# Optimization experiments

Measured on AMD Instinct MI355X. Metric: run time of the kernel, lower is better.

The kernel has to match this reference:

```python
import jax, jax.numpy as jnp
import numpy as np

B, C, H, W = 4, 256, 64, 64
C8 = C // 8


def setup_inputs() -> dict:
    key = jax.random.key(0)
    ks = jax.random.split(key, 8)
    x = jax.random.normal(ks[0], (B, C, H, W), dtype=jnp.float32)
    valid = jax.random.uniform(ks[1], (B, 1, H, W), dtype=jnp.float32)
    # 1x1 conv weights (kernel_size=1 -> plain channel matmul) + biases
    Wq = jax.random.normal(ks[2], (C8, C), dtype=jnp.float32) * 0.05
    bq = jnp.zeros((C8,), dtype=jnp.float32)
    Wk = jax.random.normal(ks[3], (C8, C), dtype=jnp.float32) * 0.05
    bk = jnp.zeros((C8,), dtype=jnp.float32)
    Wv = jax.random.normal(ks[4], (C, C), dtype=jnp.float32) * 0.05
    bv = jnp.zeros((C,), dtype=jnp.float32)
    gamma = jnp.asarray(0.5, dtype=jnp.float32)  # nonzero so attention path matters
    return {"x": x, "valid": valid, "Wq": Wq, "bq": bq, "Wk": Wk, "bk": bk,
            "Wv": Wv, "bv": bv, "gamma": gamma}


def reference(x, valid, Wq, bq, Wk, bk, Wv, bv, gamma):
    b, c, h, w = x.shape
    n = h * w
    xf = x.reshape(b, c, n)                                   # [B,C,N]
    # valid is already at (H,W): nearest interpolate to same size is identity
    v = valid.reshape(b, 1, n)                                # [B,1,N]
    q = jnp.einsum('oc,bcn->bno', Wq, xf) + bq                # [B,N,C//8]
    k = jnp.einsum('oc,bcn->bon', Wk, xf) + bk[None, :, None] # [B,C//8,N]
    energy = jnp.einsum('bno,bom->bnm', q, k)                 # [B,N,N]
    attn = jax.nn.softmax(energy, axis=-1)
    va = attn * v                                             # mask columns
    scale = 1.0 / jnp.sum(va, axis=2, keepdims=True)          # per-row renorm
    sa = va * scale                                           # [B,N,N]
    pv = jnp.einsum('oc,bcn->bon', Wv, xf) + bv[None, :, None]  # [B,C,N]
    out = jnp.einsum('bon,bmn->bom', pv, sa)                  # bmm(V, A^T)
    out = out.reshape(b, c, h, w)
    return gamma * out + x, sa
```

## Files before the change

kernel.cpp:

```cpp
#include <hip/hip_runtime.h>

typedef unsigned short u16;
typedef unsigned int u32;
typedef __attribute__((ext_vector_type(8))) short short8;
typedef __attribute__((ext_vector_type(4))) float f32x4;
typedef __attribute__((ext_vector_type(2))) unsigned int u32x2;
typedef __attribute__((ext_vector_type(4))) unsigned int u32x4;

#define BB 4
#define CC 256
#define NT 4096
#define L2E 1.4426950408889634f

__device__ __forceinline__ float b2f(u16 v) {
    union { u32 u; float f; } c; c.u = ((u32)v) << 16; return c.f;
}
__device__ __forceinline__ u16 f2b(float f) {
    union { float f; u32 u; } c; c.f = f;
    u32 u = c.u;
    return (u16)((u + 0x7fffu + ((u >> 16) & 1u)) >> 16);
}

__global__ __launch_bounds__(256) void kproj(
    const float* __restrict__ x,
    const float* __restrict__ Wq, const float* __restrict__ bq,
    const float* __restrict__ Wk, const float* __restrict__ bk,
    const float* __restrict__ Wv, const float* __restrict__ bv,
    u16* __restrict__ qh, u16* __restrict__ ql,
    u16* __restrict__ kh, u16* __restrict__ kl,
    u16* __restrict__ pvw)
{
    __shared__ __align__(16) float lA[32][68];
    __shared__ __align__(16) float lX[32][68];
    const int mt = blockIdx.x, nt = blockIdx.y, b = blockIdx.z;
    const int t = threadIdx.x;
    const int tx = t & 15, ty = t >> 4;
    const int n0 = nt * 64;

    float acc[4][4];
    #pragma unroll
    for (int i = 0; i < 4; ++i)
        #pragma unroll
        for (int j = 0; j < 4; ++j) acc[i][j] = 0.f;

    const int rA = t >> 2, kqA = (t & 3) * 8;
    const int rgA = mt * 64 + rA;
    const float* wrow;
    if (rgA < 32)      wrow = Wq + rgA * 256;
    else if (rgA < 64) wrow = Wk + (rgA - 32) * 256;
    else               wrow = Wv + (rgA - 64) * 256;
    const int kX = t >> 3, nn8 = (t & 7) * 8;
    const float* xrow = x + ((size_t)(b * CC + kX)) * NT + n0 + nn8;

    for (int k0 = 0; k0 < 256; k0 += 32) {
        f32x4 wa = *(const f32x4*)(wrow + k0 + kqA);
        f32x4 wb = *(const f32x4*)(wrow + k0 + kqA + 4);
        f32x4 xa = *(const f32x4*)(xrow + (size_t)k0 * NT);
        f32x4 xb = *(const f32x4*)(xrow + (size_t)k0 * NT + 4);
        __syncthreads();
        #pragma unroll
        for (int j = 0; j < 4; ++j) {
            lA[kqA + j    ][rA] = wa[j];
            lA[kqA + j + 4][rA] = wb[j];
        }
        *(f32x4*)&lX[kX][nn8]     = xa;
        *(f32x4*)&lX[kX][nn8 + 4] = xb;
        __syncthreads();
        #pragma unroll
        for (int k = 0; k < 32; ++k) {
            f32x4 av  = *(const f32x4*)&lA[k][ty * 4];
            f32x4 xvv = *(const f32x4*)&lX[k][tx * 4];
            #pragma unroll
            for (int i = 0; i < 4; ++i)
                #pragma unroll
                for (int j = 0; j < 4; ++j)
                    acc[i][j] = fmaf(av[i], xvv[j], acc[i][j]);
        }
    }

    #pragma unroll
    for (int i = 0; i < 4; ++i) {
        const int rg = mt * 64 + ty * 4 + i;
        float bias;
        if (rg < 32)      bias = bq[rg];
        else if (rg < 64) bias = bk[rg - 32];
        else              bias = bv[rg - 64];
        #pragma unroll
        for (int j = 0; j < 4; ++j) {
            const int n = n0 + tx * 4 + j;
            const float val = acc[i][j] + bias;
            const u16 h = f2b(val);
            const u16 l = f2b(val - b2f(h));
            if (rg < 32) {
                const size_t idx = ((size_t)(b * NT + n)) * 32 + rg;
                qh[idx] = h; ql[idx] = l;
            } else if (rg < 64) {
                const size_t idx = ((size_t)(b * NT + n)) * 32 + (rg - 32);
                kh[idx] = h; kl[idx] = l;
            } else {
                pvw[((size_t)b * CC + (rg - 64)) * NT + n] = f2b(val);
            }
        }
    }
}

__global__ __launch_bounds__(256) void kattn(
    const u16* __restrict__ qh, const u16* __restrict__ ql,
    const u16* __restrict__ kh, const u16* __restrict__ kl,
    const float* __restrict__ valid, float* __restrict__ sa)
{
    __shared__ float sred[4][4][4];
    const int b    = blockIdx.y;
    const int lane = threadIdx.x & 63;
    const int wv   = threadIdx.x >> 6;
    const int r0   = blockIdx.x * 16;
    const int quad = lane >> 4, l16 = lane & 15;
    const int ct0  = wv * 64;

    const size_t abase = ((size_t)(b * NT + r0 + l16)) * 32 + quad * 8;
    const short8 aqh = *(const short8*)(qh + abase);
    const short8 aql = *(const short8*)(ql + abase);
    const size_t kb = (size_t)b * NT * 32 + (size_t)l16 * 32 + quad * 8;
    const float* vb = valid + b * NT + l16;
    const f32x4 zero = {0.f, 0.f, 0.f, 0.f};

    float sacc[4] = {0.f, 0.f, 0.f, 0.f};
    for (int ct = ct0; ct < ct0 + 64; ++ct) {
        short8 bh = *(const short8*)(kh + kb + (size_t)ct * 512);
        short8 bl = *(const short8*)(kl + kb + (size_t)ct * 512);
        float vcol = vb[ct * 16];
        f32x4 d = __builtin_amdgcn_mfma_f32_16x16x32_bf16(aqh, bh, zero, 0, 0, 0);
        d = __builtin_amdgcn_mfma_f32_16x16x32_bf16(aql, bh, d, 0, 0, 0);
        d = __builtin_amdgcn_mfma_f32_16x16x32_bf16(aqh, bl, d, 0, 0, 0);
        #pragma unroll
        for (int i = 0; i < 4; ++i)
            sacc[i] += vcol * exp2f(fminf(d[i], 60.f) * L2E);
    }
    #pragma unroll
    for (int i = 0; i < 4; ++i) {
        #pragma unroll
        for (int off = 1; off < 16; off <<= 1)
            sacc[i] += __shfl_xor(sacc[i], off, 64);
    }
    if (l16 == 0) {
        #pragma unroll
        for (int i = 0; i < 4; ++i) sred[wv][quad][i] = sacc[i];
    }
    __syncthreads();
    float inv[4];
    #pragma unroll
    for (int i = 0; i < 4; ++i)
        inv[i] = 1.0f / (sred[0][quad][i] + sred[1][quad][i] +
                         sred[2][quad][i] + sred[3][quad][i]);

    for (int ct = ct0; ct < ct0 + 64; ++ct) {
        short8 bh = *(const short8*)(kh + kb + (size_t)ct * 512);
        short8 bl = *(const short8*)(kl + kb + (size_t)ct * 512);
        float vcol = vb[ct * 16];
        f32x4 d = __builtin_amdgcn_mfma_f32_16x16x32_bf16(aqh, bh, zero, 0, 0, 0);
        d = __builtin_amdgcn_mfma_f32_16x16x32_bf16(aql, bh, d, 0, 0, 0);
        d = __builtin_amdgcn_mfma_f32_16x16x32_bf16(aqh, bl, d, 0, 0, 0);
        #pragma unroll
        for (int i = 0; i < 4; ++i) {
            float val = vcol * exp2f(fminf(d[i], 60.f) * L2E) * inv[i];
            sa[((size_t)(b * NT + r0 + quad * 4 + i)) * NT + ct * 16 + l16] = val;
        }
    }
}

#define KOUT_BODY(CUR, T, NXA, NXB, FTA, FTB)                                  \
  {                                                                            \
    if ((T) + 2 < 32) {                                                        \
      FTA = *(const f32x4*)(sap + (size_t)((T) + 2) * 128);                    \
      FTB = *(const f32x4*)(sap + (size_t)((T) + 2) * 128 + 4);                \
    }                                                                          \
    if ((T) + 1 < 32) {                                                        \
      u32 w0 = (u32)f2b(NXA[0]) | ((u32)f2b(NXA[1]) << 16);                    \
      u32 w1 = (u32)f2b(NXA[2]) | ((u32)f2b(NXA[3]) << 16);                    \
      u32 w2 = (u32)f2b(NXB[0]) | ((u32)f2b(NXB[1]) << 16);                    \
      u32 w3 = (u32)f2b(NXB[2]) | ((u32)f2b(NXB[3]) << 16);                    \
      u32x4 pk = {w0, w1, w2, w3};                                             \
      *(u32x4*)(lbw + ((((T) + 1) & 1) * 8192)) = pk;                          \
    }                                                                          \
    const char* lb = lbr + (CUR) * 8192;                                       \
    _Pragma("unroll")                                                          \
    for (int kk = 0; kk < 128; kk += 32) {                                     \
      short8 a0 = *(const short8*)(a0p + (size_t)(T) * 128 + kk);              \
      short8 a1 = *(const short8*)(a1p + (size_t)(T) * 128 + kk);              \
      const int kby = (((kk + quad * 8) * 2) ^ swz);                           \
      short8 b0 = *(const short8*)(lb + l16 * 256 + kby);                      \
      short8 b1 = *(const short8*)(lb + (16 + l16) * 256 + kby);               \
      acc00 = __builtin_amdgcn_mfma_f32_16x16x32_bf16(a0, b0, acc00, 0, 0, 0); \
      acc01 = __builtin_amdgcn_mfma_f32_16x16x32_bf16(a0, b1, acc01, 0, 0, 0); \
      acc10 = __builtin_amdgcn_mfma_f32_16x16x32_bf16(a1, b0, acc10, 0, 0, 0); \
      acc11 = __builtin_amdgcn_mfma_f32_16x16x32_bf16(a1, b1, acc11, 0, 0, 0); \
    }                                                                          \
    asm volatile("s_waitcnt lgkmcnt(0)" ::: "memory");                         \
    __builtin_amdgcn_sched_barrier(0);                                         \
    __builtin_amdgcn_s_barrier();                                              \
    __builtin_amdgcn_sched_barrier(0);                                         \
  }

__global__ __launch_bounds__(512) void kout(
    const u16* __restrict__ pvw, const float* __restrict__ sa,
    const float* __restrict__ x, const float* __restrict__ gamma,
    float* __restrict__ outp)
{
    __shared__ __align__(16) u16 lB[2][32][128];
    const int b    = blockIdx.y;
    const int m0   = blockIdx.x * 32;
    const int t    = threadIdx.x;
    const int lane = t & 63;
    const int wv   = t >> 6;
    const int c0   = wv * 32;
    const int quad = lane >> 4, l16 = lane & 15;
    const int swz  = (l16 & 7) << 4;

    const u16* a0p = pvw + ((size_t)(b * CC + c0 + l16)) * NT + quad * 8;
    const u16* a1p = a0p + (size_t)16 * NT;
    const int sm = t >> 4, sk = (t & 15) * 8;
    const float* sap = sa + ((size_t)(b * NT + m0 + sm)) * NT + sk;
    char* lbw = ((char*)&lB[0][0][0]) + sm * 256 + ((sk * 2) ^ ((sm & 7) << 4));
    const char* lbr = (const char*)&lB[0][0][0];

    f32x4 acc00 = {0,0,0,0}, acc01 = {0,0,0,0}, acc10 = {0,0,0,0}, acc11 = {0,0,0,0};

    f32x4 pA = *(const f32x4*)(sap);
    f32x4 pB = *(const f32x4*)(sap + 4);
    f32x4 nA = *(const f32x4*)(sap + 128);
    f32x4 nB = *(const f32x4*)(sap + 132);
    {
        u32 w0 = (u32)f2b(pA[0]) | ((u32)f2b(pA[1]) << 16);
        u32 w1 = (u32)f2b(pA[2]) | ((u32)f2b(pA[3]) << 16);
        u32 w2 = (u32)f2b(pB[0]) | ((u32)f2b(pB[1]) << 16);
        u32 w3 = (u32)f2b(pB[2]) | ((u32)f2b(pB[3]) << 16);
        u32x4 pk = {w0, w1, w2, w3};
        *(u32x4*)(lbw) = pk;
    }
    asm volatile("s_waitcnt lgkmcnt(0)" ::: "memory");
    __builtin_amdgcn_sched_barrier(0);
    __builtin_amdgcn_s_barrier();
    __builtin_amdgcn_sched_barrier(0);

    f32x4 fA, fB;
    for (int tt = 0; tt < 32; tt += 2) {
        KOUT_BODY(0, tt,     nA, nB, fA, fB)
        KOUT_BODY(1, tt + 1, fA, fB, nA, nB)
    }

    const float g = gamma[0];
    #pragma unroll
    for (int ai = 0; ai < 2; ++ai) {
        #pragma unroll
        for (int bi = 0; bi < 2; ++bi) {
            f32x4 acc = (ai == 0) ? ((bi == 0) ? acc00 : acc01)
                                  : ((bi == 0) ? acc10 : acc11);
            #pragma unroll
            for (int i = 0; i < 4; ++i) {
                const int c = c0 + ai * 16 + quad * 4 + i;
                const int m = m0 + bi * 16 + l16;
                const size_t idx = ((size_t)(b * CC + c)) * NT + m;
                outp[idx] = g * acc[i] + x[idx];
            }
        }
    }
}

extern "C" void kernel_launch(void* const* d_in, const int* in_sizes, int n_in,
                              void* d_out, int out_size, void* d_ws, size_t ws_size,
                              hipStream_t stream)
{
    const float* x     = (const float*)d_in[0];
    const float* valid = (const float*)d_in[1];
    const float* Wq    = (const float*)d_in[2];
    const float* bq    = (const float*)d_in[3];
    const float* Wk    = (const float*)d_in[4];
    const float* bk    = (const float*)d_in[5];
    const float* Wv    = (const float*)d_in[6];
    const float* bv    = (const float*)d_in[7];
    const float* gamma = (const float*)d_in[8];

    float* outp = (float*)d_out;
    float* sa   = outp + (size_t)BB * CC * NT;

    u16* qh  = (u16*)d_ws;
    u16* ql  = qh + (size_t)BB * NT * 32;
    u16* kh  = ql + (size_t)BB * NT * 32;
    u16* kl  = kh + (size_t)BB * NT * 32;
    u16* pvw = kl + (size_t)BB * NT * 32;

    kproj<<<dim3(5, 64, BB), 256, 0, stream>>>(x, Wq, bq, Wk, bk, Wv, bv,
                                               qh, ql, kh, kl, pvw);
    kattn<<<dim3(256, BB), 256, 0, stream>>>(qh, ql, kh, kl, valid, sa);
    kout<<<dim3(128, BB), 512, 0, stream>>>(pvw, sa, x, gamma, outp);
}
```

Baseline: 534.5 us.

## Compute QKV projection with split-bf16 MFMA and pre-split weights

Adds a prep kernel that splits the fused Wq/Wk/Wv weights into bf16 hi/lo halves and gathers the biases. The projection kernel now loads a full 256x64 x tile into LDS and computes all 320 output rows with 16x16x32 bf16 MFMA using three hi/lo products for near-fp32 accuracy. This replaces scalar fp32 FMA tiling and writes q/k in vectorised packed form. It adds an extra launch, uses heavy register and LDS usage at one block per CU, and produces a smaller grid.

```diff
diff --git a/kernel.cpp b/kernel.cpp
--- a/kernel.cpp
+++ b/kernel.cpp
@@ -21,84 +21,132 @@
     return (u16)((u + 0x7fffu + ((u >> 16) & 1u)) >> 16);
 }
 
-__global__ __launch_bounds__(256) void kproj(
+__global__ __launch_bounds__(256) void kprep(
+    const float* __restrict__ Wq, const float* __restrict__ Wk,
+    const float* __restrict__ Wv, const float* __restrict__ bq,
+    const float* __restrict__ bk_, const float* __restrict__ bv,
+    u16* __restrict__ wh, u16* __restrict__ wl, float* __restrict__ biasAll)
+{
+    const int bkx = blockIdx.x;
+    const int t = threadIdx.x;
+    #pragma unroll
+    for (int j = 0; j < 4; ++j) {
+        const int idx4 = t + 256 * j;
+        const int row  = bkx * 16 + (idx4 >> 6);
+        const int col4 = (idx4 & 63) * 4;
+        const float* src = row < 32 ? Wq + row * 256
+                         : row < 64 ? Wk + (row - 32) * 256
+                         :            Wv + (row - 64) * 256;
+        f32x4 v = *(const f32x4*)(src + col4);
+        u16 h[4], l[4];
+        #pragma unroll
+        for (int i = 0; i < 4; ++i) {
+            h[i] = f2b(v[i]);
+            l[i] = f2b(v[i] - b2f(h[i]));
+        }
+        u32x2 ph, pl;
+        ph[0] = (u32)h[0] | ((u32)h[1] << 16); ph[1] = (u32)h[2] | ((u32)h[3] << 16);
+        pl[0] = (u32)l[0] | ((u32)l[1] << 16); pl[1] = (u32)l[2] | ((u32)l[3] << 16);
+        *(u32x2*)(wh + row * 256 + col4) = ph;
+        *(u32x2*)(wl + row * 256 + col4) = pl;
+    }
+    if (t < 16) {
+        const int row = bkx * 16 + t;
+        biasAll[row] = row < 32 ? bq[row] : row < 64 ? bk_[row - 32] : bv[row - 64];
+    }
+}
+
+__global__ __launch_bounds__(256, 1) void kproj(
     const float* __restrict__ x,
-    const float* __restrict__ Wq, const float* __restrict__ bq,
-    const float* __restrict__ Wk, const float* __restrict__ bk,
-    const float* __restrict__ Wv, const float* __restrict__ bv,
+    const u16* __restrict__ wh, const u16* __restrict__ wl,
+    const float* __restrict__ biasAll,
     u16* __restrict__ qh, u16* __restrict__ ql,
     u16* __restrict__ kh, u16* __restrict__ kl,
     u16* __restrict__ pvw)
 {
-    __shared__ __align__(16) float lA[32][68];
-    __shared__ __align__(16) float lX[32][68];
-    const int mt = blockIdx.x, nt = blockIdx.y, b = blockIdx.z;
+    __shared__ __align__(16) float lX[256][68];
+    __shared__ float lbias[320];
+    const int b = blockIdx.y, n0 = blockIdx.x * 64;
     const int t = threadIdx.x;
-    const int tx = t & 15, ty = t >> 4;
-    const int n0 = nt * 64;
-
-    float acc[4][4];
-    #pragma unroll
-    for (int i = 0; i < 4; ++i)
-        #pragma unroll
-        for (int j = 0; j < 4; ++j) acc[i][j] = 0.f;
-
-    const int rA = t >> 2, kqA = (t & 3) * 8;
-    const int rgA = mt * 64 + rA;
-    const float* wrow;
-    if (rgA < 32)      wrow = Wq + rgA * 256;
-    else if (rgA < 64) wrow = Wk + (rgA - 32) * 256;
-    else               wrow = Wv + (rgA - 64) * 256;
-    const int kX = t >> 3, nn8 = (t & 7) * 8;
-    const float* xrow = x + ((size_t)(b * CC + kX)) * NT + n0 + nn8;
-
-    for (int k0 = 0; k0 < 256; k0 += 32) {
-        f32x4 wa = *(const f32x4*)(wrow + k0 + kqA);
-        f32x4 wb = *(const f32x4*)(wrow + k0 + kqA + 4);
-        f32x4 xa = *(const f32x4*)(xrow + (size_t)k0 * NT);
-        f32x4 xb = *(const f32x4*)(xrow + (size_t)k0 * NT + 4);
-        __syncthreads();
-        #pragma unroll
-        for (int j = 0; j < 4; ++j) {
-            lA[kqA + j    ][rA] = wa[j];
-            lA[kqA + j + 4][rA] = wb[j];
-        }
-        *(f32x4*)&lX[kX][nn8]     = xa;
-        *(f32x4*)&lX[kX][nn8 + 4] = xb;
-        __syncthreads();
-        #pragma unroll
-        for (int k = 0; k < 32; ++k) {
-            f32x4 av  = *(const f32x4*)&lA[k][ty * 4];
-            f32x4 xvv = *(const f32x4*)&lX[k][tx * 4];
+    const int lane = t & 63, wv = t >> 6;
+    const int quad = lane >> 4, l16 = lane & 15;
+
+    {
+        const int kX = t >> 3, nn8 = (t & 7) * 8;
+        const float* xrow = x + ((size_t)(b * CC + kX)) * NT + n0 + nn8;
+        #pragma unroll
+        for (int k0 = 0; k0 < 256; k0 += 32) {
+            f32x4 xa = *(const f32x4*)(xrow + (size_t)k0 * NT);
+            f32x4 xb = *(const f32x4*)(xrow + (size_t)k0 * NT + 4);
+            *(f32x4*)&lX[k0 + kX][nn8]     = xa;
+            *(f32x4*)&lX[k0 + kX][nn8 + 4] = xb;
+        }
+        lbias[t] = biasAll[t];
+        if (t < 64) lbias[256 + t] = biasAll[256 + t];
+    }
+    __syncthreads();
+
+    short8 bh[8], bl[8];
+    const int coln = wv * 16 + l16;
+    #pragma unroll
+    for (int s = 0; s < 8; ++s) {
+        #pragma unroll
+        for (int e = 0; e < 8; ++e) {
+            float v = lX[s * 32 + quad * 8 + e][coln];
+            u16 h = f2b(v);
+            bh[s][e] = (short)h;
+            bl[s][e] = (short)f2b(v - b2f(h));
+        }
+    }
+
+    f32x4 acc[20];
+    #pragma unroll
+    for (int mt = 0; mt < 20; ++mt) acc[mt] = (f32x4){0.f, 0.f, 0.f, 0.f};
+
+    const u16* whp = wh + l16 * 256 + quad * 8;
+    const u16* wlp = wl + l16 * 256 + quad * 8;
+    #pragma unroll
+    for (int mt = 0; mt < 20; ++mt) {
+        #pragma unroll
+        for (int s = 0; s < 8; ++s) {
+            short8 ah = *(const short8*)(whp + mt * 4096 + s * 32);
+            short8 al = *(const short8*)(wlp + mt * 4096 + s * 32);
+            acc[mt] = __builtin_amdgcn_mfma_f32_16x16x32_bf16(ah, bh[s], acc[mt], 0, 0, 0);
+            acc[mt] = __builtin_amdgcn_mfma_f32_16x16x32_bf16(al, bh[s], acc[mt], 0, 0, 0);
+            acc[mt] = __builtin_amdgcn_mfma_f32_16x16x32_bf16(ah, bl[s], acc[mt], 0, 0, 0);
+        }
+    }
+
+    const int n = n0 + wv * 16 + l16;
+    #pragma unroll
+    for (int mt = 0; mt < 20; ++mt) {
+        u16 hv[4], lv[4];
+        #pragma unroll
+        for (int i = 0; i < 4; ++i) {
+            const int o = mt * 16 + quad * 4 + i;
+            const float val = acc[mt][i] + lbias[o];
+            hv[i] = f2b(val);
+            lv[i] = f2b(val - b2f(hv[i]));
+        }
+        if (mt < 2) {
+            u32x2 ph, pl;
+            ph[0] = (u32)hv[0] | ((u32)hv[1] << 16); ph[1] = (u32)hv[2] | ((u32)hv[3] << 16);
+            pl[0] = (u32)lv[0] | ((u32)lv[1] << 16); pl[1] = (u32)lv[2] | ((u32)lv[3] << 16);
+            const size_t idx = ((size_t)(b * NT + n)) * 32 + mt * 16 + quad * 4;
+            *(u32x2*)(qh + idx) = ph;
+            *(u32x2*)(ql + idx) = pl;
+        } else if (mt < 4) {
+            u32x2 ph, pl;
+            ph[0] = (u32)hv[0] | ((u32)hv[1] << 16); ph[1] = (u32)hv[2] | ((u32)hv[3] << 16);
+            pl[0] = (u32)lv[0] | ((u32)lv[1] << 16); pl[1] = (u32)lv[2] | ((u32)lv[3] << 16);
+            const size_t idx = ((size_t)(b * NT + n)) * 32 + (mt - 2) * 16 + quad * 4;
+            *(u32x2*)(kh + idx) = ph;
+            *(u32x2*)(kl + idx) = pl;
+        } else {
             #pragma unroll
-            for (int i = 0; i < 4; ++i)
-                #pragma unroll
-                for (int j = 0; j < 4; ++j)
-                    acc[i][j] = fmaf(av[i], xvv[j], acc[i][j]);
-        }
-    }
-
-    #pragma unroll
-    for (int i = 0; i < 4; ++i) {
-        const int rg = mt * 64 + ty * 4 + i;
-        float bias;
-        if (rg < 32)      bias = bq[rg];
-        else if (rg < 64) bias = bk[rg - 32];
-        else              bias = bv[rg - 64];
-        #pragma unroll
-        for (int j = 0; j < 4; ++j) {
-            const int n = n0 + tx * 4 + j;
-            const float val = acc[i][j] + bias;
-            const u16 h = f2b(val);
-            const u16 l = f2b(val - b2f(h));
-            if (rg < 32) {
-                const size_t idx = ((size_t)(b * NT + n)) * 32 + rg;
-                qh[idx] = h; ql[idx] = l;
-            } else if (rg < 64) {
-                const size_t idx = ((size_t)(b * NT + n)) * 32 + (rg - 32);
-                kh[idx] = h; kl[idx] = l;
-            } else {
-                pvw[((size_t)b * CC + (rg - 64)) * NT + n] = f2b(val);
+            for (int i = 0; i < 4; ++i) {
+                const int c = mt * 16 + quad * 4 + i - 64;
+                pvw[((size_t)(b * CC + c)) * NT + n] = hv[i];
             }
         }
     }
@@ -288,9 +336,13 @@
     u16* kh  = ql + (size_t)BB * NT * 32;
     u16* kl  = kh + (size_t)BB * NT * 32;
     u16* pvw = kl + (size_t)BB * NT * 32;
-
-    kproj<<<dim3(5, 64, BB), 256, 0, stream>>>(x, Wq, bq, Wk, bk, Wv, bv,
-                                               qh, ql, kh, kl, pvw);
+    u16* wh  = pvw + (size_t)BB * CC * NT;
+    u16* wl  = wh + 320 * 256;
+    float* biasAll = (float*)(wl + 320 * 256);
+
+    kprep<<<dim3(20), 256, 0, stream>>>(Wq, Wk, Wv, bq, bk, bv, wh, wl, biasAll);
+    kproj<<<dim3(64, BB), 256, 0, stream>>>(x, wh, wl, biasAll,
+                                            qh, ql, kh, kl, pvw);
     kattn<<<dim3(256, BB), 256, 0, stream>>>(qh, ql, kh, kl, valid, sa);
     kout<<<dim3(128, BB), 512, 0, stream>>>(pvw, sa, x, gamma, outp);
 }
```

Result: no change. 545.0 us (+2.0%).
